# Performance work log

Hardware: AMD Instinct MI355X
Metric: run time of the kernel (lower is better)

## Reference

```python
import jax, jax.numpy as jnp
import numpy as np

W0_SIREN = 30.0  # omega_0 used in sine activations

HID = [64, 64, 256, 256, 256]
IN_DIM = 65   # 64 feat channels + 1 time channel
OUT_DIM = 64


def _siren_params(key):
    dims = [IN_DIM] + HID + [OUT_DIM]
    params = []
    for i in range(len(dims) - 1):
        fan_in, fan_out = dims[i], dims[i + 1]
        key, kw, kb = jax.random.split(key, 3)
        if i == 0:
            bound = 1.0 / fan_in
        else:
            bound = np.sqrt(6.0 / fan_in) / W0_SIREN
        W = jax.random.uniform(kw, (fan_out, fan_in), jnp.float32, -bound, bound)
        b = jax.random.uniform(kb, (fan_out,), jnp.float32, -bound, bound)
        params.append((W, b))
    return params


def setup_inputs() -> dict:
    key = jax.random.key(0)
    k_feat, k_t, k_p = jax.random.split(key, 3)
    feat = jax.random.normal(k_feat, (2, 64, 192, 320), jnp.float32)
    times = jax.random.uniform(k_t, (3,), jnp.float32)
    params = _siren_params(k_p)
    inp = {"feat": feat, "times": times}
    for i, (W, b) in enumerate(params):
        inp[f"w{i}"] = W
        inp[f"b{i}"] = b
    return inp


def _gather_full_grid(feat):
    """Nearest grid_sample (align_corners=False) at pixel-center coords over the full grid.
    Returns [B, H*W, C]."""
    B, C, H, W = feat.shape
    # make_coord pixel centers in [-1, 1]
    ys = -1.0 + (2.0 * jnp.arange(H, dtype=jnp.float32) + 1.0) / H
    xs = -1.0 + (2.0 * jnp.arange(W, dtype=jnp.float32) + 1.0) / W
    gy, gx = jnp.meshgrid(ys, xs, indexing="ij")          # [H, W] each
    gy, gx = gy.reshape(-1), gx.reshape(-1)               # [qs]
    # grid_sample nearest, align_corners=False unnormalization
    iy = jnp.clip(jnp.round(((gy + 1.0) * H - 1.0) / 2.0).astype(jnp.int32), 0, H - 1)
    ix = jnp.clip(jnp.round(((gx + 1.0) * W - 1.0) / 2.0).astype(jnp.int32), 0, W - 1)
    q = feat[:, :, iy, ix]                                # [B, C, qs] gather
    return jnp.transpose(q, (0, 2, 1))                    # [B, qs, C]


def _siren_mlp(x, ws, bs):
    h = x
    n = len(ws)
    for i in range(n - 1):
        h = jnp.sin(W0_SIREN * (h @ ws[i].T + bs[i]))
    return h @ ws[n - 1].T + bs[n - 1]                    # outermost linear


def reference(feat, times, w0, b0, w1, b1, w2, b2, w3, b3, w4, b4, w5, b5):
    ws = [w0, w1, w2, w3, w4, w5]
    bs = [b0, b1, b2, b3, b4, b5]
    B, C, H, W = feat.shape
    qs = H * W
    q_feat = _gather_full_grid(feat)                      # [B, qs, 64]
    preds = []
    for c in range(3):  # Training==True branch: 3 time stamps
        t = times[c]
        pe = jnp.full((B, qs, 1), 1.0, feat.dtype) * t    # time channel
        enc = jnp.concatenate([q_feat, pe], axis=-1)      # [B, qs, 65]
        out = _siren_mlp(enc.reshape(B * qs, IN_DIM), ws, bs)  # [B*qs, 64]
        # F.fold with kernel_size=1 == reshape back to spatial map
        pred = out.reshape(B, qs, OUT_DIM).transpose(0, 2, 1).reshape(B, OUT_DIM, H, W)
        preds.append(pred)
    return jnp.stack(preds, axis=0)                       # [3, B, 64, H, W]
```

## Files before the change

### kernel.cpp

```cpp
#include <hip/hip_runtime.h>
#include <hip/hip_bf16.h>

typedef __bf16 bf16_t;
typedef bf16_t bf16x8 __attribute__((ext_vector_type(8)));
typedef float f32x4 __attribute__((ext_vector_type(4)));
typedef unsigned short u16;
typedef unsigned int u32;

static constexpr int kHW = 192 * 320;
static constexpr float kC = 4.77464829275686f;

__device__ __forceinline__ u16 f2bf(float f) {
  u32 u = __float_as_uint(f);
  return (u16)((u + 0x7FFFu + ((u >> 16) & 1u)) >> 16);
}

__device__ __forceinline__ u32 pack2(float a, float b) {
  __hip_bfloat162 h = __float22bfloat162_rn(make_float2(a, b));
  union { __hip_bfloat162 h2; u32 u; } cv;
  cv.h2 = h;
  return cv.u;
}

__device__ __forceinline__ void lds_barrier() {
  __asm__ volatile("s_waitcnt lgkmcnt(0)\n\ts_barrier" ::: "memory");
}

static constexpr int OFF_W0 = 0;
static constexpr int OFF_W1 = 4096;
static constexpr int OFF_W2 = 8192;
static constexpr int OFF_W3 = 24576;
static constexpr int OFF_W4 = 90112;
static constexpr int OFF_W5 = 155648;
static constexpr int W_TOTAL = 172032;
static constexpr int B_TOTAL = 1024;
static constexpr size_t FEAT_BYTE_OFF = 348160;
static constexpr size_t WS_NEED = FEAT_BYTE_OFF + (size_t)1920 * 8192;

__global__ void convert_weights(const float* __restrict__ w0, const float* __restrict__ w1,
                                const float* __restrict__ w2, const float* __restrict__ w3,
                                const float* __restrict__ w4, const float* __restrict__ w5,
                                const float* __restrict__ b0, const float* __restrict__ b1,
                                const float* __restrict__ b2, const float* __restrict__ b3,
                                const float* __restrict__ b4, const float* __restrict__ b5,
                                u16* __restrict__ wb, float* __restrict__ bws) {
  int i = blockIdx.x * 256 + threadIdx.x;
  if (i < W_TOTAL) {
    float v, s = kC;
    if (i < OFF_W1)      { int o = i >> 6, k = i & 63; v = w0[o * 65 + k]; }
    else if (i < OFF_W2) { v = w1[i - OFF_W1]; }
    else if (i < OFF_W3) { v = w2[i - OFF_W2]; }
    else if (i < OFF_W4) { v = w3[i - OFF_W3]; }
    else if (i < OFF_W5) { v = w4[i - OFF_W4]; }
    else                 { v = w5[i - OFF_W5]; s = 1.0f; }
    wb[i] = f2bf(v * s);
  } else {
    int j = i - W_TOTAL;
    float v;
    if (j < 64)       v = kC * b0[j];
    else if (j < 128) v = kC * w0[(j - 64) * 65 + 64];
    else if (j < 192) v = kC * b1[j - 128];
    else if (j < 448) v = kC * b2[j - 192];
    else if (j < 704) v = kC * b3[j - 448];
    else if (j < 960) v = kC * b4[j - 704];
    else              v = b5[j - 960];
    bws[j] = v;
  }
}

__global__ void convert_feat(const float* __restrict__ feat, u16* __restrict__ featT) {
  const int chunk = blockIdx.x;
  const int bq  = chunk / 960;
  const int hw0 = (chunk % 960) * 64;
  const int tid = threadIdx.x;
  const int p   = tid & 63;
  const int gg  = tid >> 6;
  const float* fbase = feat + (size_t)bq * 64 * kHW + hw0 + p;
  u16* img = featT + (size_t)chunk * 4096;
#pragma unroll
  for (int j = 0; j < 2; ++j) {
    const int g = gg * 2 + j;
    float v[8];
#pragma unroll
    for (int e = 0; e < 8; ++e) v[e] = fbase[(size_t)(g * 8 + e) * kHW];
    uint4 pk;
    pk.x = pack2(v[0], v[1]);
    pk.y = pack2(v[2], v[3]);
    pk.z = pack2(v[4], v[5]);
    pk.w = pack2(v[6], v[7]);
    *reinterpret_cast<uint4*>(img + p * 64 + ((g ^ (p & 7)) * 8)) = pk;
  }
}

template<int RSO>
__device__ __forceinline__ void epilogue_sin(f32x4 acc, u16* outb, int p, int g,
                                             int quad, int sw) {
  float s0 = __builtin_amdgcn_sinf(__builtin_amdgcn_fractf(acc[0]));
  float s1 = __builtin_amdgcn_sinf(__builtin_amdgcn_fractf(acc[1]));
  float s2 = __builtin_amdgcn_sinf(__builtin_amdgcn_fractf(acc[2]));
  float s3 = __builtin_amdgcn_sinf(__builtin_amdgcn_fractf(acc[3]));
  uint2 v;
  v.x = pack2(s0, s1);
  v.y = pack2(s2, s3);
  *reinterpret_cast<uint2*>(outb + p * RSO + ((g ^ sw) * 8) + (quad & 1) * 4) = v;
}

__device__ __forceinline__ f32x4 mf(bf16x8 a, bf16x8 b, f32x4 c) {
  return __builtin_amdgcn_mfma_f32_16x16x32_bf16(a, b, c, 0, 0, 0);
}

template<bool PRE>
__global__ __attribute__((amdgpu_waves_per_eu(2, 2)))
void __launch_bounds__(256)
siren_main(const float* __restrict__ feat, const float* __restrict__ times,
           const u16* __restrict__ wb, const float* __restrict__ bws,
           const u16* __restrict__ featT, float* __restrict__ out) {
  __shared__ __align__(16) u16 A32[64 * 256];
  __shared__ __align__(16) u16 B32[64 * 256];
  u16* X = B32;
  u16* Y = B32 + 4096;

  const int tid   = threadIdx.x;
  const int bid   = blockIdx.x;
  const int c     = bid / 1920;
  const int chunk = bid % 1920;
  const int bq    = chunk / 960;
  const int hw0   = (chunk % 960) * 64;
  const float t   = times[c];
  const int wave  = tid >> 6;
  const int lane  = tid & 63;
  const int l15   = lane & 15;
  const int quad  = lane >> 4;
  const int sw    = l15 & 7;

  auto read_af8 = [&](bf16x8 (&af)[8], const u16* in, int pt) {
#pragma unroll
    for (int ks = 0; ks < 8; ++ks)
      af[ks] = *reinterpret_cast<const bf16x8*>(
          in + (pt * 16 + l15) * 256 + (((ks * 4 + quad) ^ sw) * 8));
  };
  auto read_af2 = [&](bf16x8 (&af)[2], const u16* in, int pt) {
#pragma unroll
    for (int ks = 0; ks < 2; ++ks)
      af[ks] = *reinterpret_cast<const bf16x8*>(
          in + (pt * 16 + l15) * 64 + (((ks * 4 + quad) ^ sw) * 8));
  };
  auto load_wf_half = [&](bf16x8 (&wf)[4][4], const u16* wbase, int kh) {
#pragma unroll
    for (int ks = 0; ks < 4; ++ks)
#pragma unroll
      for (int ot = 0; ot < 4; ++ot)
        wf[ot][ks] = *reinterpret_cast<const bf16x8*>(
            wbase + ((wave * 4 + ot) * 16 + l15) * 256 + (kh * 4 + ks) * 32 + quad * 8);
  };
  auto load_bv4 = [&](f32x4 (&bv)[4], const float* bg) {
#pragma unroll
    for (int ot = 0; ot < 4; ++ot)
      bv[ot] = *reinterpret_cast<const f32x4*>(bg + (wave * 4 + ot) * 16 + quad * 4);
  };
  auto mfma_pt = [&](f32x4 (&acc)[4], bf16x8 (&wa)[4][4], bf16x8 (&wbh)[4][4],
                     bf16x8 (&af)[8], const f32x4 (&bv)[4]) {
#pragma unroll
    for (int ot = 0; ot < 4; ++ot) acc[ot] = bv[ot];
#pragma unroll
    for (int ks = 0; ks < 8; ++ks)
#pragma unroll
      for (int ot = 0; ot < 4; ++ot)
        acc[ot] = mf(ks < 4 ? wa[ot][ks] : wbh[ot][ks - 4], af[ks], acc[ot]);
  };
  auto epi_pt4 = [&](f32x4 (&acc)[4], u16* outb, int pt) {
#pragma unroll
    for (int ot = 0; ot < 4; ++ot)
      epilogue_sin<256>(acc[ot], outb, pt * 16 + l15,
                        (wave * 4 + ot) * 2 + (quad >> 1), quad, sw);
  };

  bf16x8 wf0[2], wf1[2];
#pragma unroll
  for (int ks = 0; ks < 2; ++ks) {
    wf0[ks] = *reinterpret_cast<const bf16x8*>(wb + OFF_W0 + (wave * 16 + l15) * 64 + ks * 32 + quad * 8);
    wf1[ks] = *reinterpret_cast<const bf16x8*>(wb + OFF_W1 + (wave * 16 + l15) * 64 + ks * 32 + quad * 8);
  }
  f32x4 bv0, bv1;
  {
    f32x4 cb = *reinterpret_cast<const f32x4*>(bws + wave * 16 + quad * 4);
    f32x4 cw = *reinterpret_cast<const f32x4*>(bws + 64 + wave * 16 + quad * 4);
#pragma unroll
    for (int r = 0; r < 4; ++r) bv0[r] = cb[r] + t * cw[r];
    bv1 = *reinterpret_cast<const f32x4*>(bws + 128 + wave * 16 + quad * 4);
  }

  bf16x8 wf2[4][2];
  f32x4  bv2[4];

  if constexpr (PRE) {
    const u16* fsrc = featT + (size_t)chunk * 4096;
    bf16x8 a0[2], a1[2];
    auto rdg = [&](bf16x8 (&a)[2], int pt) {
#pragma unroll
      for (int ks = 0; ks < 2; ++ks)
        a[ks] = *reinterpret_cast<const bf16x8*>(
            fsrc + (pt * 16 + l15) * 64 + (((ks * 4 + quad) ^ sw) * 8));
    };
    rdg(a0, 0);
    rdg(a1, 1);
#pragma unroll
    for (int ks = 0; ks < 2; ++ks)
#pragma unroll
      for (int ot = 0; ot < 4; ++ot)
        wf2[ot][ks] = *reinterpret_cast<const bf16x8*>(
            wb + OFF_W2 + ((wave * 4 + ot) * 16 + l15) * 64 + ks * 32 + quad * 8);
    load_bv4(bv2, bws + 192);

    f32x4 acc;
    acc = bv0; acc = mf(wf0[0], a0[0], acc); acc = mf(wf0[1], a0[1], acc);
    rdg(a0, 2);
    epilogue_sin<64>(acc, Y, 0 * 16 + l15, wave * 2 + (quad >> 1), quad, sw);
    acc = bv0; acc = mf(wf0[0], a1[0], acc); acc = mf(wf0[1], a1[1], acc);
    rdg(a1, 3);
    epilogue_sin<64>(acc, Y, 1 * 16 + l15, wave * 2 + (quad >> 1), quad, sw);
    acc = bv0; acc = mf(wf0[0], a0[0], acc); acc = mf(wf0[1], a0[1], acc);
    epilogue_sin<64>(acc, Y, 2 * 16 + l15, wave * 2 + (quad >> 1), quad, sw);
    acc = bv0; acc = mf(wf0[0], a1[0], acc); acc = mf(wf0[1], a1[1], acc);
    epilogue_sin<64>(acc, Y, 3 * 16 + l15, wave * 2 + (quad >> 1), quad, sw);
  } else {
    {
      const int p  = tid & 63;
      const int gg = tid >> 6;
      const float* fbase = feat + (size_t)bq * 64 * kHW + hw0 + p;
#pragma unroll
      for (int j = 0; j < 2; ++j) {
        const int g = gg * 2 + j;
        float v[8];
#pragma unroll
        for (int e = 0; e < 8; ++e) v[e] = fbase[(size_t)(g * 8 + e) * kHW];
        uint4 pk;
        pk.x = pack2(v[0], v[1]);
        pk.y = pack2(v[2], v[3]);
        pk.z = pack2(v[4], v[5]);
        pk.w = pack2(v[6], v[7]);
        *reinterpret_cast<uint4*>(X + p * 64 + ((g ^ (p & 7)) * 8)) = pk;
      }
    }
    lds_barrier();
#pragma unroll
    for (int ks = 0; ks < 2; ++ks)
#pragma unroll
      for (int ot = 0; ot < 4; ++ot)
        wf2[ot][ks] = *reinterpret_cast<const bf16x8*>(
            wb + OFF_W2 + ((wave * 4 + ot) * 16 + l15) * 64 + ks * 32 + quad * 8);
    load_bv4(bv2, bws + 192);
#pragma unroll
    for (int pt = 0; pt < 4; ++pt) {
      bf16x8 a[2];
      read_af2(a, X, pt);
      f32x4 acc = bv0;
      acc = mf(wf0[0], a[0], acc); acc = mf(wf0[1], a[1], acc);
      epilogue_sin<64>(acc, Y, pt * 16 + l15, wave * 2 + (quad >> 1), quad, sw);
    }
  }
  lds_barrier();

  bf16x8 wf3a[4][4], wf3b[4][4];
  f32x4  bv3[4];
  {
    bf16x8 a0[2], a1[2];
    read_af2(a0, Y, 0);
    read_af2(a1, Y, 1);
    load_wf_half(wf3a, wb + OFF_W3, 0);
    load_bv4(bv3, bws + 448);
    f32x4 acc;
    acc = bv1; acc = mf(wf1[0], a0[0], acc); acc = mf(wf1[1], a0[1], acc);
    read_af2(a0, Y, 2);
    epilogue_sin<64>(acc, X, 0 * 16 + l15, wave * 2 + (quad >> 1), quad, sw);
    acc = bv1; acc = mf(wf1[0], a1[0], acc); acc = mf(wf1[1], a1[1], acc);
    read_af2(a1, Y, 3);
    epilogue_sin<64>(acc, X, 1 * 16 + l15, wave * 2 + (quad >> 1), quad, sw);
    acc = bv1; acc = mf(wf1[0], a0[0], acc); acc = mf(wf1[1], a0[1], acc);
    epilogue_sin<64>(acc, X, 2 * 16 + l15, wave * 2 + (quad >> 1), quad, sw);
    acc = bv1; acc = mf(wf1[0], a1[0], acc); acc = mf(wf1[1], a1[1], acc);
    epilogue_sin<64>(acc, X, 3 * 16 + l15, wave * 2 + (quad >> 1), quad, sw);
  }
  lds_barrier();

  {
    bf16x8 a0[2], a1[2];
    read_af2(a0, X, 0);
    read_af2(a1, X, 1);
    {
      f32x4 acc[4];
#pragma unroll
      for (int ot = 0; ot < 4; ++ot) {
        acc[ot] = bv2[ot];
        acc[ot] = mf(wf2[ot][0], a0[0], acc[ot]);
        acc[ot] = mf(wf2[ot][1], a0[1], acc[ot]);
      }
      read_af2(a0, X, 2);
      epi_pt4(acc, A32, 0);
    }
    {
      f32x4 acc[4];
#pragma unroll
      for (int ot = 0; ot < 4; ++ot) {
        acc[ot] = bv2[ot];
        acc[ot] = mf(wf2[ot][0], a1[0], acc[ot]);
        acc[ot] = mf(wf2[ot][1], a1[1], acc[ot]);
      }
      read_af2(a1, X, 3);
      epi_pt4(acc, A32, 1);
    }
    {
      f32x4 acc[4];
#pragma unroll
      for (int ot = 0; ot < 4; ++ot) {
        acc[ot] = bv2[ot];
        acc[ot] = mf(wf2[ot][0], a0[0], acc[ot]);
        acc[ot] = mf(wf2[ot][1], a0[1], acc[ot]);
      }
      load_wf_half(wf3b, wb + OFF_W3, 1);
      epi_pt4(acc, A32, 2);
    }
    {
      f32x4 acc[4];
#pragma unroll
      for (int ot = 0; ot < 4; ++ot) {
        acc[ot] = bv2[ot];
        acc[ot] = mf(wf2[ot][0], a1[0], acc[ot]);
        acc[ot] = mf(wf2[ot][1], a1[1], acc[ot]);
      }
      epi_pt4(acc, A32, 3);
    }
  }
  lds_barrier();

  bf16x8 wf4a[4][4], wf4b[4][4];
  f32x4  bv4[4];
  {
    bf16x8 afA[8], afB[8];
    read_af8(afA, A32, 0);
    read_af8(afB, A32, 1);
    {
      f32x4 acc[4];
      mfma_pt(acc, wf3a, wf3b, afA, bv3);
      read_af8(afA, A32, 2);
      epi_pt4(acc, B32, 0);
    }
    {
      f32x4 acc[4];
      mfma_pt(acc, wf3a, wf3b, afB, bv3);
      read_af8(afB, A32, 3);
      epi_pt4(acc, B32, 1);
    }
    {
      f32x4 acc[4];
      mfma_pt(acc, wf3a, wf3b, afA, bv3);
      epi_pt4(acc, B32, 2);
    }
    {
      f32x4 acc[4];
      mfma_pt(acc, wf3a, wf3b, afB, bv3);
      load_wf_half(wf4a, wb + OFF_W4, 0);
      load_bv4(bv4, bws + 704);
      epi_pt4(acc, B32, 3);
    }
  }
  lds_barrier();

  bf16x8 wf5[8];
  f32x4  bv5;
  {
    load_wf_half(wf4b, wb + OFF_W4, 1);
    bf16x8 afA[8], afB[8];
    read_af8(afA, B32, 0);
    read_af8(afB, B32, 1);
    {
      f32x4 acc[4];
      mfma_pt(acc, wf4a, wf4b, afA, bv4);
      read_af8(afA, B32, 2);
      epi_pt4(acc, A32, 0);
    }
    {
      f32x4 acc[4];
      mfma_pt(acc, wf4a, wf4b, afB, bv4);
      read_af8(afB, B32, 3);
      epi_pt4(acc, A32, 1);
    }
    {
      f32x4 acc[4];
      mfma_pt(acc, wf4a, wf4b, afA, bv4);
      epi_pt4(acc, A32, 2);
    }
    {
      f32x4 acc[4];
      mfma_pt(acc, wf4a, wf4b, afB, bv4);
#pragma unroll
      for (int ks = 0; ks < 8; ++ks)
        wf5[ks] = *reinterpret_cast<const bf16x8*>(
            wb + OFF_W5 + (wave * 16 + l15) * 256 + ks * 32 + quad * 8);
      bv5 = *reinterpret_cast<const f32x4*>(bws + 960 + wave * 16 + quad * 4);
      epi_pt4(acc, A32, 3);
    }
  }
  lds_barrier();

  {
    float* out_base = out + (size_t)(c * 2 + bq) * 64 * kHW + hw0;
    bf16x8 afA[8], afB[8];
    read_af8(afA, A32, 0);
    read_af8(afB, A32, 1);
#pragma unroll
    for (int pt = 0; pt < 4; ++pt) {
      bf16x8 (&af)[8] = (pt & 1) ? afB : afA;
      f32x4 acc = bv5;
#pragma unroll
      for (int ks = 0; ks < 8; ++ks) acc = mf(wf5[ks], af[ks], acc);
      if (pt == 0) read_af8(afA, A32, 2);
      if (pt == 1) read_af8(afB, A32, 3);
      const int p = pt * 16 + l15;
      const int o = wave * 16 + quad * 4;
      float* dst = out_base + (size_t)o * kHW + p;
#pragma unroll
      for (int r = 0; r < 4; ++r) dst[(size_t)r * kHW] = acc[r];
    }
  }
}

extern "C" void kernel_launch(void* const* d_in, const int* in_sizes, int n_in,
                              void* d_out, int out_size, void* d_ws, size_t ws_size,
                              hipStream_t stream) {
  const float* feat  = (const float*)d_in[0];
  const float* times = (const float*)d_in[1];
  const float* w0 = (const float*)d_in[2];
  const float* b0 = (const float*)d_in[3];
  const float* w1 = (const float*)d_in[4];
  const float* b1 = (const float*)d_in[5];
  const float* w2 = (const float*)d_in[6];
  const float* b2 = (const float*)d_in[7];
  const float* w3 = (const float*)d_in[8];
  const float* b3 = (const float*)d_in[9];
  const float* w4 = (const float*)d_in[10];
  const float* b4 = (const float*)d_in[11];
  const float* w5 = (const float*)d_in[12];
  const float* b5 = (const float*)d_in[13];
  u16*   wb  = (u16*)d_ws;
  float* bws = (float*)((char*)d_ws + (size_t)W_TOTAL * 2);
  float* out = (float*)d_out;

  convert_weights<<<(W_TOTAL + B_TOTAL) / 256, 256, 0, stream>>>(
      w0, w1, w2, w3, w4, w5, b0, b1, b2, b3, b4, b5, wb, bws);

  if (ws_size >= WS_NEED) {
    u16* featT = (u16*)((char*)d_ws + FEAT_BYTE_OFF);
    convert_feat<<<1920, 256, 0, stream>>>(feat, featT);
    siren_main<true><<<5760, 256, 0, stream>>>(feat, times, wb, bws, featT, out);
  } else {
    siren_main<false><<<5760, 256, 0, stream>>>(feat, times, wb, bws, wb, out);
  }
}
```

Before: 392.9 us.

## Split SIREN block work across 8 waves with 512 threads per block

Doubles the block from 4 to 8 waves. In the 256-wide layers each wave now owns 2 output tiles instead of 4, and in the 64-wide layers each wave handles half of the 64 points. This cuts per-wave register pressure for weight fragments (wf3/wf4 hold 2x8 fragments instead of two 4x4 halves), which is meant to raise latency hiding through more waves per SIMD. The cost is that each weight fragment is loaded by more waves overall, and the 256-wide layers lose some of the A-fragment reuse they had with 4 tiles per wave.

```diff
diff --git a/kernel.cpp b/kernel.cpp
--- a/kernel.cpp
+++ b/kernel.cpp
@@ -110,8 +110,8 @@
 }
 
 template<bool PRE>
-__global__ __attribute__((amdgpu_waves_per_eu(2, 2)))
-void __launch_bounds__(256)
+__global__ __attribute__((amdgpu_waves_per_eu(4, 4)))
+void __launch_bounds__(512)
 siren_main(const float* __restrict__ feat, const float* __restrict__ times,
            const u16* __restrict__ wb, const float* __restrict__ bws,
            const u16* __restrict__ featT, float* __restrict__ out) {
@@ -132,6 +132,9 @@
   const int l15   = lane & 15;
   const int quad  = lane >> 4;
   const int sw    = l15 & 7;
+  const int wlo   = wave & 3;
+  const int whi   = wave >> 2;
+  const int p0    = whi * 2;
 
   auto read_af8 = [&](bf16x8 (&af)[8], const u16* in, int pt) {
 #pragma unroll
@@ -145,279 +148,235 @@
       af[ks] = *reinterpret_cast<const bf16x8*>(
           in + (pt * 16 + l15) * 64 + (((ks * 4 + quad) ^ sw) * 8));
   };
-  auto load_wf_half = [&](bf16x8 (&wf)[4][4], const u16* wbase, int kh) {
-#pragma unroll
-    for (int ks = 0; ks < 4; ++ks)
-#pragma unroll
-      for (int ot = 0; ot < 4; ++ot)
+  auto load_wf8 = [&](bf16x8 (&wf)[2][8], const u16* wbase) {
+#pragma unroll
+    for (int ot = 0; ot < 2; ++ot)
+#pragma unroll
+      for (int ks = 0; ks < 8; ++ks)
         wf[ot][ks] = *reinterpret_cast<const bf16x8*>(
-            wbase + ((wave * 4 + ot) * 16 + l15) * 256 + (kh * 4 + ks) * 32 + quad * 8);
-  };
-  auto load_bv4 = [&](f32x4 (&bv)[4], const float* bg) {
-#pragma unroll
-    for (int ot = 0; ot < 4; ++ot)
-      bv[ot] = *reinterpret_cast<const f32x4*>(bg + (wave * 4 + ot) * 16 + quad * 4);
-  };
-  auto mfma_pt = [&](f32x4 (&acc)[4], bf16x8 (&wa)[4][4], bf16x8 (&wbh)[4][4],
-                     bf16x8 (&af)[8], const f32x4 (&bv)[4]) {
-#pragma unroll
-    for (int ot = 0; ot < 4; ++ot) acc[ot] = bv[ot];
+            wbase + ((wave * 2 + ot) * 16 + l15) * 256 + ks * 32 + quad * 8);
+  };
+  auto load_bv2 = [&](f32x4 (&bv)[2], const float* bg) {
+#pragma unroll
+    for (int ot = 0; ot < 2; ++ot)
+      bv[ot] = *reinterpret_cast<const f32x4*>(bg + (wave * 2 + ot) * 16 + quad * 4);
+  };
+  auto mfma_pt2 = [&](f32x4 (&acc)[2], bf16x8 (&wf)[2][8], bf16x8 (&af)[8],
+                      const f32x4 (&bv)[2]) {
+#pragma unroll
+    for (int ot = 0; ot < 2; ++ot) acc[ot] = bv[ot];
 #pragma unroll
     for (int ks = 0; ks < 8; ++ks)
 #pragma unroll
-      for (int ot = 0; ot < 4; ++ot)
-        acc[ot] = mf(ks < 4 ? wa[ot][ks] : wbh[ot][ks - 4], af[ks], acc[ot]);
-  };
-  auto epi_pt4 = [&](f32x4 (&acc)[4], u16* outb, int pt) {
-#pragma unroll
-    for (int ot = 0; ot < 4; ++ot)
+      for (int ot = 0; ot < 2; ++ot)
+        acc[ot] = mf(wf[ot][ks], af[ks], acc[ot]);
+  };
+  auto epi_pt2 = [&](f32x4 (&acc)[2], u16* outb, int pt) {
+#pragma unroll
+    for (int ot = 0; ot < 2; ++ot)
       epilogue_sin<256>(acc[ot], outb, pt * 16 + l15,
-                        (wave * 4 + ot) * 2 + (quad >> 1), quad, sw);
+                        (wave * 2 + ot) * 2 + (quad >> 1), quad, sw);
   };
 
   bf16x8 wf0[2], wf1[2];
 #pragma unroll
   for (int ks = 0; ks < 2; ++ks) {
-    wf0[ks] = *reinterpret_cast<const bf16x8*>(wb + OFF_W0 + (wave * 16 + l15) * 64 + ks * 32 + quad * 8);
-    wf1[ks] = *reinterpret_cast<const bf16x8*>(wb + OFF_W1 + (wave * 16 + l15) * 64 + ks * 32 + quad * 8);
+    wf0[ks] = *reinterpret_cast<const bf16x8*>(wb + OFF_W0 + (wlo * 16 + l15) * 64 + ks * 32 + quad * 8);
+    wf1[ks] = *reinterpret_cast<const bf16x8*>(wb + OFF_W1 + (wlo * 16 + l15) * 64 + ks * 32 + quad * 8);
   }
   f32x4 bv0, bv1;
   {
-    f32x4 cb = *reinterpret_cast<const f32x4*>(bws + wave * 16 + quad * 4);
-    f32x4 cw = *reinterpret_cast<const f32x4*>(bws + 64 + wave * 16 + quad * 4);
+    f32x4 cb = *reinterpret_cast<const f32x4*>(bws + wlo * 16 + quad * 4);
+    f32x4 cw = *reinterpret_cast<const f32x4*>(bws + 64 + wlo * 16 + quad * 4);
 #pragma unroll
     for (int r = 0; r < 4; ++r) bv0[r] = cb[r] + t * cw[r];
-    bv1 = *reinterpret_cast<const f32x4*>(bws + 128 + wave * 16 + quad * 4);
-  }
-
-  bf16x8 wf2[4][2];
-  f32x4  bv2[4];
+    bv1 = *reinterpret_cast<const f32x4*>(bws + 128 + wlo * 16 + quad * 4);
+  }
+
+  bf16x8 wf2[2][2];
+  f32x4  bv2[2];
 
   if constexpr (PRE) {
     const u16* fsrc = featT + (size_t)chunk * 4096;
     bf16x8 a0[2], a1[2];
-    auto rdg = [&](bf16x8 (&a)[2], int pt) {
+#pragma unroll
+    for (int ks = 0; ks < 2; ++ks) {
+      a0[ks] = *reinterpret_cast<const bf16x8*>(
+          fsrc + (p0 * 16 + l15) * 64 + (((ks * 4 + quad) ^ sw) * 8));
+      a1[ks] = *reinterpret_cast<const bf16x8*>(
+          fsrc + ((p0 + 1) * 16 + l15) * 64 + (((ks * 4 + quad) ^ sw) * 8));
+    }
+#pragma unroll
+    for (int ot = 0; ot < 2; ++ot)
 #pragma unroll
       for (int ks = 0; ks < 2; ++ks)
-        a[ks] = *reinterpret_cast<const bf16x8*>(
-            fsrc + (pt * 16 + l15) * 64 + (((ks * 4 + quad) ^ sw) * 8));
-    };
-    rdg(a0, 0);
-    rdg(a1, 1);
-#pragma unroll
-    for (int ks = 0; ks < 2; ++ks)
-#pragma unroll
-      for (int ot = 0; ot < 4; ++ot)
         wf2[ot][ks] = *reinterpret_cast<const bf16x8*>(
-            wb + OFF_W2 + ((wave * 4 + ot) * 16 + l15) * 64 + ks * 32 + quad * 8);
-    load_bv4(bv2, bws + 192);
+            wb + OFF_W2 + ((wave * 2 + ot) * 16 + l15) * 64 + ks * 32 + quad * 8);
+    load_bv2(bv2, bws + 192);
 
     f32x4 acc;
     acc = bv0; acc = mf(wf0[0], a0[0], acc); acc = mf(wf0[1], a0[1], acc);
-    rdg(a0, 2);
-    epilogue_sin<64>(acc, Y, 0 * 16 + l15, wave * 2 + (quad >> 1), quad, sw);
+    epilogue_sin<64>(acc, Y, p0 * 16 + l15, wlo * 2 + (quad >> 1), quad, sw);
     acc = bv0; acc = mf(wf0[0], a1[0], acc); acc = mf(wf0[1], a1[1], acc);
-    rdg(a1, 3);
-    epilogue_sin<64>(acc, Y, 1 * 16 + l15, wave * 2 + (quad >> 1), quad, sw);
-    acc = bv0; acc = mf(wf0[0], a0[0], acc); acc = mf(wf0[1], a0[1], acc);
-    epilogue_sin<64>(acc, Y, 2 * 16 + l15, wave * 2 + (quad >> 1), quad, sw);
-    acc = bv0; acc = mf(wf0[0], a1[0], acc); acc = mf(wf0[1], a1[1], acc);
-    epilogue_sin<64>(acc, Y, 3 * 16 + l15, wave * 2 + (quad >> 1), quad, sw);
+    epilogue_sin<64>(acc, Y, (p0 + 1) * 16 + l15, wlo * 2 + (quad >> 1), quad, sw);
   } else {
     {
       const int p  = tid & 63;
-      const int gg = tid >> 6;
+      const int g  = tid >> 6;
       const float* fbase = feat + (size_t)bq * 64 * kHW + hw0 + p;
-#pragma unroll
-      for (int j = 0; j < 2; ++j) {
-        const int g = gg * 2 + j;
-        float v[8];
-#pragma unroll
-        for (int e = 0; e < 8; ++e) v[e] = fbase[(size_t)(g * 8 + e) * kHW];
-        uint4 pk;
-        pk.x = pack2(v[0], v[1]);
-        pk.y = pack2(v[2], v[3]);
-        pk.z = pack2(v[4], v[5]);
-        pk.w = pack2(v[6], v[7]);
-        *reinterpret_cast<uint4*>(X + p * 64 + ((g ^ (p & 7)) * 8)) = pk;
-      }
+      float v[8];
+#pragma unroll
+      for (int e = 0; e < 8; ++e) v[e] = fbase[(size_t)(g * 8 + e) * kHW];
+      uint4 pk;
+      pk.x = pack2(v[0], v[1]);
+      pk.y = pack2(v[2], v[3]);
+      pk.z = pack2(v[4], v[5]);
+      pk.w = pack2(v[6], v[7]);
+      *reinterpret_cast<uint4*>(X + p * 64 + ((g ^ (p & 7)) * 8)) = pk;
     }
     lds_barrier();
 #pragma unroll
-    for (int ks = 0; ks < 2; ++ks)
-#pragma unroll
-      for (int ot = 0; ot < 4; ++ot)
+    for (int ot = 0; ot < 2; ++ot)
+#pragma unroll
+      for (int ks = 0; ks < 2; ++ks)
         wf2[ot][ks] = *reinterpret_cast<const bf16x8*>(
-            wb + OFF_W2 + ((wave * 4 + ot) * 16 + l15) * 64 + ks * 32 + quad * 8);
-    load_bv4(bv2, bws + 192);
-#pragma unroll
-    for (int pt = 0; pt < 4; ++pt) {
+            wb + OFF_W2 + ((wave * 2 + ot) * 16 + l15) * 64 + ks * 32 + quad * 8);
+    load_bv2(bv2, bws + 192);
+#pragma unroll
+    for (int i = 0; i < 2; ++i) {
       bf16x8 a[2];
-      read_af2(a, X, pt);
+      read_af2(a, X, p0 + i);
       f32x4 acc = bv0;
       acc = mf(wf0[0], a[0], acc); acc = mf(wf0[1], a[1], acc);
-      epilogue_sin<64>(acc, Y, pt * 16 + l15, wave * 2 + (quad >> 1), quad, sw);
+      epilogue_sin<64>(acc, Y, (p0 + i) * 16 + l15, wlo * 2 + (quad >> 1), quad, sw);
     }
   }
   lds_barrier();
 
-  bf16x8 wf3a[4][4], wf3b[4][4];
-  f32x4  bv3[4];
   {
     bf16x8 a0[2], a1[2];
-    read_af2(a0, Y, 0);
-    read_af2(a1, Y, 1);
-    load_wf_half(wf3a, wb + OFF_W3, 0);
-    load_bv4(bv3, bws + 448);
+    read_af2(a0, Y, p0);
+    read_af2(a1, Y, p0 + 1);
     f32x4 acc;
     acc = bv1; acc = mf(wf1[0], a0[0], acc); acc = mf(wf1[1], a0[1], acc);
-    read_af2(a0, Y, 2);
-    epilogue_sin<64>(acc, X, 0 * 16 + l15, wave * 2 + (quad >> 1), quad, sw);
+    epilogue_sin<64>(acc, X, p0 * 16 + l15, wlo * 2 + (quad >> 1), quad, sw);
     acc = bv1; acc = mf(wf1[0], a1[0], acc); acc = mf(wf1[1], a1[1], acc);
-    read_af2(a1, Y, 3);
-    epilogue_sin<64>(acc, X, 1 * 16 + l15, wave * 2 + (quad >> 1), quad, sw);
-    acc = bv1; acc = mf(wf1[0], a0[0], acc); acc = mf(wf1[1], a0[1], acc);
-    epilogue_sin<64>(acc, X, 2 * 16 + l15, wave * 2 + (quad >> 1), quad, sw);
-    acc = bv1; acc = mf(wf1[0], a1[0], acc); acc = mf(wf1[1], a1[1], acc);
-    epilogue_sin<64>(acc, X, 3 * 16 + l15, wave * 2 + (quad >> 1), quad, sw);
+    epilogue_sin<64>(acc, X, (p0 + 1) * 16 + l15, wlo * 2 + (quad >> 1), quad, sw);
   }
   lds_barrier();
 
+  bf16x8 wf3[2][8];
+  f32x4  bv3[2];
   {
     bf16x8 a0[2], a1[2];
     read_af2(a0, X, 0);
     read_af2(a1, X, 1);
     {
-      f32x4 acc[4];
-#pragma unroll
-      for (int ot = 0; ot < 4; ++ot) {
+      f32x4 acc[2];
+#pragma unroll
+      for (int ot = 0; ot < 2; ++ot) {
         acc[ot] = bv2[ot];
         acc[ot] = mf(wf2[ot][0], a0[0], acc[ot]);
         acc[ot] = mf(wf2[ot][1], a0[1], acc[ot]);
       }
       read_af2(a0, X, 2);
-      epi_pt4(acc, A32, 0);
+      epi_pt2(acc, A32, 0);
     }
     {
-      f32x4 acc[4];
-#pragma unroll
-      for (int ot = 0; ot < 4; ++ot) {
+      f32x4 acc[2];
+#pragma unroll
+      for (int ot = 0; ot < 2; ++ot) {
         acc[ot] = bv2[ot];
         acc[ot] = mf(wf2[ot][0], a1[0], acc[ot]);
         acc[ot] = mf(wf2[ot][1], a1[1], acc[ot]);
       }
       read_af2(a1, X, 3);
-      epi_pt4(acc, A32, 1);
+      epi_pt2(acc, A32, 1);
     }
     {
-      f32x4 acc[4];
-#pragma unroll
-      for (int ot = 0; ot < 4; ++ot) {
+      f32x4 acc[2];
+#pragma unroll
+      for (int ot = 0; ot < 2; ++ot) {
         acc[ot] = bv2[ot];
         acc[ot] = mf(wf2[ot][0], a0[0], acc[ot]);
         acc[ot] = mf(wf2[ot][1], a0[1], acc[ot]);
       }
-      load_wf_half(wf3b, wb + OFF_W3, 1);
-      epi_pt4(acc, A32, 2);
+      epi_pt2(acc, A32, 2);
     }
     {
-      f32x4 acc[4];
-#pragma unroll
-      for (int ot = 0; ot < 4; ++ot) {
+      f32x4 acc[2];
+#pragma unroll
+      for (int ot = 0; ot < 2; ++ot) {
         acc[ot] = bv2[ot];
         acc[ot] = mf(wf2[ot][0], a1[0], acc[ot]);
         acc[ot] = mf(wf2[ot][1], a1[1], acc[ot]);
       }
-      epi_pt4(acc, A32, 3);
+      load_wf8(wf3, wb + OFF_W3);
+      load_bv2(bv3, bws + 448);
+      epi_pt2(acc, A32, 3);
     }
   }
   lds_barrier();
 
-  bf16x8 wf4a[4][4], wf4b[4][4];
-  f32x4  bv4[4];
-  {
-    bf16x8 afA[8], afB[8];
-    read_af8(afA, A32, 0);
-    read_af8(afB, A32, 1);
-    {
-      f32x4 acc[4];
-      mfma_pt(acc, wf3a, wf3b, afA, bv3);
-      read_af8(afA, A32, 2);
-      epi_pt4(acc, B32, 0);
-    }
-    {
-      f32x4 acc[4];
-      mfma_pt(acc, wf3a, wf3b, afB, bv3);
-      read_af8(afB, A32, 3);
-      epi_pt4(acc, B32, 1);
-    }
-    {
-      f32x4 acc[4];
-      mfma_pt(acc, wf3a, wf3b, afA, bv3);
-      epi_pt4(acc, B32, 2);
-    }
-    {
-      f32x4 acc[4];
-      mfma_pt(acc, wf3a, wf3b, afB, bv3);
-      load_wf_half(wf4a, wb + OFF_W4, 0);
-      load_bv4(bv4, bws + 704);
-      epi_pt4(acc, B32, 3);
-    }
+  bf16x8 wf4[2][8];
+  f32x4  bv4[2];
+  {
+    bf16x8 af[8];
+    f32x4 acc[2];
+    read_af8(af, A32, 0);
+    mfma_pt2(acc, wf3, af, bv3);
+    read_af8(af, A32, 1);
+    epi_pt2(acc, B32, 0);
+    mfma_pt2(acc, wf3, af, bv3);
+    read_af8(af, A32, 2);
+    epi_pt2(acc, B32, 1);
+    mfma_pt2(acc, wf3, af, bv3);
+    read_af8(af, A32, 3);
+    epi_pt2(acc, B32, 2);
+    mfma_pt2(acc, wf3, af, bv3);
+    load_wf8(wf4, wb + OFF_W4);
+    load_bv2(bv4, bws + 704);
+    epi_pt2(acc, B32, 3);
   }
   lds_barrier();
 
   bf16x8 wf5[8];
   f32x4  bv5;
   {
-    load_wf_half(wf4b, wb + OFF_W4, 1);
-    bf16x8 afA[8], afB[8];
-    read_af8(afA, B32, 0);
-    read_af8(afB, B32, 1);
-    {
-      f32x4 acc[4];
-      mfma_pt(acc, wf4a, wf4b, afA, bv4);
-      read_af8(afA, B32, 2);
-      epi_pt4(acc, A32, 0);
-    }
-    {
-      f32x4 acc[4];
-      mfma_pt(acc, wf4a, wf4b, afB, bv4);
-      read_af8(afB, B32, 3);
-      epi_pt4(acc, A32, 1);
-    }
-    {
-      f32x4 acc[4];
-      mfma_pt(acc, wf4a, wf4b, afA, bv4);
-      epi_pt4(acc, A32, 2);
-    }
-    {
-      f32x4 acc[4];
-      mfma_pt(acc, wf4a, wf4b, afB, bv4);
-#pragma unroll
-      for (int ks = 0; ks < 8; ++ks)
-        wf5[ks] = *reinterpret_cast<const bf16x8*>(
-            wb + OFF_W5 + (wave * 16 + l15) * 256 + ks * 32 + quad * 8);
-      bv5 = *reinterpret_cast<const f32x4*>(bws + 960 + wave * 16 + quad * 4);
-      epi_pt4(acc, A32, 3);
-    }
+    bf16x8 af[8];
+    f32x4 acc[2];
+    read_af8(af, B32, 0);
+    mfma_pt2(acc, wf4, af, bv4);
+    read_af8(af, B32, 1);
+    epi_pt2(acc, A32, 0);
+    mfma_pt2(acc, wf4, af, bv4);
+    read_af8(af, B32, 2);
+    epi_pt2(acc, A32, 1);
+    mfma_pt2(acc, wf4, af, bv4);
+    read_af8(af, B32, 3);
+    epi_pt2(acc, A32, 2);
+    mfma_pt2(acc, wf4, af, bv4);
+#pragma unroll
+    for (int ks = 0; ks < 8; ++ks)
+      wf5[ks] = *reinterpret_cast<const bf16x8*>(
+          wb + OFF_W5 + (wlo * 16 + l15) * 256 + ks * 32 + quad * 8);
+    bv5 = *reinterpret_cast<const f32x4*>(bws + 960 + wlo * 16 + quad * 4);
+    epi_pt2(acc, A32, 3);
   }
   lds_barrier();
 
   {
     float* out_base = out + (size_t)(c * 2 + bq) * 64 * kHW + hw0;
-    bf16x8 afA[8], afB[8];
-    read_af8(afA, A32, 0);
-    read_af8(afB, A32, 1);
-#pragma unroll
-    for (int pt = 0; pt < 4; ++pt) {
-      bf16x8 (&af)[8] = (pt & 1) ? afB : afA;
+    bf16x8 af[8];
+#pragma unroll
+    for (int i = 0; i < 2; ++i) {
+      const int pt = p0 + i;
+      read_af8(af, A32, pt);
       f32x4 acc = bv5;
 #pragma unroll
       for (int ks = 0; ks < 8; ++ks) acc = mf(wf5[ks], af[ks], acc);
-      if (pt == 0) read_af8(afA, A32, 2);
-      if (pt == 1) read_af8(afB, A32, 3);
       const int p = pt * 16 + l15;
-      const int o = wave * 16 + quad * 4;
+      const int o = wlo * 16 + quad * 4;
       float* dst = out_base + (size_t)o * kHW + p;
 #pragma unroll
       for (int r = 0; r < 4; ++r) dst[(size_t)r * kHW] = acc[r];
@@ -452,8 +411,8 @@
   if (ws_size >= WS_NEED) {
     u16* featT = (u16*)((char*)d_ws + FEAT_BYTE_OFF);
     convert_feat<<<1920, 256, 0, stream>>>(feat, featT);
-    siren_main<true><<<5760, 256, 0, stream>>>(feat, times, wb, bws, featT, out);
+    siren_main<true><<<5760, 512, 0, stream>>>(feat, times, wb, bws, featT, out);
   } else {
-    siren_main<false><<<5760, 256, 0, stream>>>(feat, times, wb, bws, wb, out);
-  }
-}
+    siren_main<false><<<5760, 512, 0, stream>>>(feat, times, wb, bws, wb, out);
+  }
+}
```

Result: slower. 426.8 us (+8.6%).
